# Kernel tuning notes

Measured on AMD Instinct MI355X. Metric: run time of the kernel, lower is better.

The kernel has to match this reference:

```python
import math
import jax, jax.numpy as jnp
import numpy as np

NUM_BUCKETS = 32
MAX_DISTANCE = 128
N_HEADS = 16
D_KV = 64


def _relative_position_bucket(rel_pos):
    # encoder (bidirectional) path of UMT5Attention._relative_position_bucket
    num_buckets = NUM_BUCKETS // 2
    rel_buckets = (rel_pos > 0).astype(jnp.int32) * num_buckets
    rel_pos = jnp.abs(rel_pos)
    max_exact = num_buckets // 2
    is_small = rel_pos < max_exact
    # clamp to 1 inside log only to avoid nan; those entries are masked by is_small
    rel_pos_large = max_exact + (
        jnp.log(jnp.maximum(rel_pos, 1).astype(jnp.float32) / max_exact)
        / math.log(MAX_DISTANCE / max_exact)
        * (num_buckets - max_exact)
    ).astype(jnp.int32)
    rel_pos_large = jnp.minimum(rel_pos_large, num_buckets - 1)
    return rel_buckets + jnp.where(is_small, rel_pos, rel_pos_large)


def compute_bias(rel_bias, q_len, k_len):
    ctx = jnp.arange(q_len, dtype=jnp.int32)[:, None]
    mem = jnp.arange(k_len, dtype=jnp.int32)[None, :]
    bkt = _relative_position_bucket(mem - ctx)          # [q, k]
    values = rel_bias[bkt]                               # [q, k, H]
    return jnp.transpose(values, (2, 0, 1))[None]        # [1, H, q, k]


def setup_inputs() -> dict:
    key = jax.random.key(0)
    ks = jax.random.split(key, 6)
    B, S, D = 2, 2048, 1024
    s = 1.0 / math.sqrt(D)
    return {
        "hidden_states": jax.random.normal(ks[0], (B, S, D), jnp.float32),
        "attention_mask": jnp.ones((B, S), jnp.int32),
        "Wq": jax.random.normal(ks[1], (D, D), jnp.float32) * s,
        "Wk": jax.random.normal(ks[2], (D, D), jnp.float32) * s,
        "Wv": jax.random.normal(ks[3], (D, D), jnp.float32) * s,
        "Wo": jax.random.normal(ks[4], (D, D), jnp.float32) * s,
        "rel_bias": jax.random.normal(ks[5], (NUM_BUCKETS, N_HEADS), jnp.float32),
    }


def reference(hidden_states, attention_mask, Wq, Wk, Wv, Wo, rel_bias):
    b, s, _ = hidden_states.shape
    n, c = N_HEADS, D_KV
    q = (hidden_states @ Wq).reshape(b, s, n, c)
    k = (hidden_states @ Wk).reshape(b, s, n, c)
    v = (hidden_states @ Wv).reshape(b, s, n, c)
    position_bias = compute_bias(rel_bias, s, s)          # [1, H, s, s]
    mask = attention_mask[:, None, None, :]               # [b, 1, 1, s]
    position_bias = jnp.where(mask == 0,
                              jnp.finfo(hidden_states.dtype).min,
                              position_bias)
    # T5-style: no 1/sqrt(d) query scaling
    attn = jnp.einsum('binc,bjnc->bnij', q, k) + position_bias
    attn = jax.nn.softmax(attn, axis=-1)
    o = jnp.einsum('bnij,bjnc->binc', attn, v).reshape(b, s, n * c)
    return o @ Wo
```

## Files before the change

### kernel.cpp

```cpp
#include <hip/hip_runtime.h>
#include <hip/hip_bf16.h>

#define NH 16
#define DC 64
#define SEQ 2048
#define BATCH 2
#define DM 1024
#define MTOT (BATCH*SEQ)

#define LOG2E 1.44269504f
#define SMAX_BOUND 48.0f

typedef unsigned short u16;
typedef unsigned int u32;
typedef __bf16 bf16x8 __attribute__((ext_vector_type(8)));
typedef float f32x4 __attribute__((ext_vector_type(4)));
typedef int i32x4 __attribute__((ext_vector_type(4)));
typedef unsigned u32x2v __attribute__((ext_vector_type(2)));

struct __attribute__((packed, aligned(4))) f4u { f32x4 v; };

__device__ __forceinline__ u16 f2bf(float f) {
    unsigned int x = __float_as_uint(f);
    unsigned int r = (x + 0x7fffu + ((x >> 16) & 1u)) >> 16;
    return (u16)r;
}
__device__ __forceinline__ u32 cvtpk(float a, float b) {
    u32 r;
    asm("v_cvt_pk_bf16_f32 %0, %1, %2" : "=v"(r) : "v"(a), "v"(b));
    return r;
}

__device__ __forceinline__ f32x4 mfma16(bf16x8 a, bf16x8 b, f32x4 c) {
    return __builtin_amdgcn_mfma_f32_16x16x32_bf16(a, b, c, 0, 0, 0);
}

__device__ __forceinline__ void glds(const u16* g, u16* l) {
    __builtin_amdgcn_global_load_lds(
        (const __attribute__((address_space(1))) void*)g,
        (__attribute__((address_space(3))) void*)l, 16, 0, 0);
}

__device__ __forceinline__ float psum32(float v) {
    u32x2v t = __builtin_amdgcn_permlane32_swap(__float_as_uint(v), __float_as_uint(v), false, false);
    return __uint_as_float(t.x) + __uint_as_float(t.y);
}
__device__ __forceinline__ float psum16(float v) {
    u32x2v t = __builtin_amdgcn_permlane16_swap(__float_as_uint(v), __float_as_uint(v), false, false);
    return __uint_as_float(t.x) + __uint_as_float(t.y);
}


__global__ void convert_hs(const float* __restrict__ src, u16* __restrict__ dst, int n4) {
    int idx = blockIdx.x * blockDim.x + threadIdx.x;
    int stride = gridDim.x * blockDim.x;
    for (int i = idx; i < n4; i += stride) {
        float4 v = reinterpret_cast<const float4*>(src)[i];
        uint2 o;
        o.x = (unsigned)f2bf(v.x) | ((unsigned)f2bf(v.y) << 16);
        o.y = (unsigned)f2bf(v.z) | ((unsigned)f2bf(v.w) << 16);
        reinterpret_cast<uint2*>(dst)[i] = o;
    }
}

__global__ void wtrans(const float* __restrict__ Wq, const float* __restrict__ Wk,
                       const float* __restrict__ Wv, const float* __restrict__ Wo,
                       u16* __restrict__ wT) {
    int z = blockIdx.z;
    const float* W = (z == 0) ? Wq : (z == 1) ? Wk : (z == 2) ? Wv : Wo;
    float sc = (z == 0) ? LOG2E : 1.0f;
    u16* WT = wT + (size_t)z * DM * DM;
    __shared__ float tile[32][33];
    int tx = threadIdx.x, ty = threadIdx.y;
    int kbase = blockIdx.y * 32, nbase = blockIdx.x * 32;
#pragma unroll
    for (int i = 0; i < 4; i++)
        tile[ty * 4 + i][tx] = W[(size_t)(kbase + ty * 4 + i) * DM + nbase + tx];
    __syncthreads();
#pragma unroll
    for (int i = 0; i < 4; i++)
        WT[(size_t)(nbase + ty * 4 + i) * DM + kbase + tx] = f2bf(tile[tx][ty * 4 + i] * sc);
}

__global__ void bias_table(const float* __restrict__ rel_bias, float* __restrict__ tab) {
    int idx = blockIdx.x * blockDim.x + threadIdx.x;
    if (idx >= NH * 2 * SEQ) return;
    int n = idx >> 12;
    int dpos = idx & 4095;
    int delta = dpos - 2048;
    int rb = (delta > 0) ? 16 : 0;
    int a = (delta < 0) ? -delta : delta;
    int ib;
    if (a < 8) {
        ib = a;
    } else {
        ib = 8 + (int)(logf((float)a / 8.0f) / logf(16.0f) * 8.0f);
        if (ib > 15) ib = 15;
    }
    tab[idx] = (rel_bias[(rb + ib) * NH + n] - SMAX_BOUND) * LOG2E;
}

__global__ __launch_bounds__(256) void vtrans(const u16* __restrict__ V, u16* __restrict__ VT) {
    int st = blockIdx.x;
    int hb = blockIdx.y;
    const u16* src = V + ((size_t)hb * SEQ + st * 64) * DC;
    u16* dst = VT + (size_t)hb * DC * SEQ + st * 64;
    __shared__ u16 t[64][65];
    int tid = threadIdx.x;
    int r = tid >> 2, c0 = (tid & 3) * 16;
    union { bf16x8 v; u16 s[8]; } a0, a1;
    a0.v = *reinterpret_cast<const bf16x8*>(src + (size_t)r * DC + c0);
    a1.v = *reinterpret_cast<const bf16x8*>(src + (size_t)r * DC + c0 + 8);
#pragma unroll
    for (int j = 0; j < 8; j++) { t[r][c0 + j] = a0.s[j]; t[r][c0 + 8 + j] = a1.s[j]; }
    __syncthreads();
    int c = tid >> 2, s0 = (tid & 3) * 16;
    union { bf16x8 v; u16 s[8]; } o0, o1;
#pragma unroll
    for (int j = 0; j < 8; j++) { o0.s[j] = t[s0 + j][c]; o1.s[j] = t[s0 + 8 + j][c]; }
    *reinterpret_cast<bf16x8*>(dst + (size_t)c * SEQ + s0)     = o0.v;
    *reinterpret_cast<bf16x8*>(dst + (size_t)c * SEQ + s0 + 8) = o1.v;
}


template<int MODE>
__global__ __launch_bounds__(256) void gemm_bt(
    const u16* __restrict__ A, const u16* __restrict__ BT,
    u16* __restrict__ qkvout, float* __restrict__ fout)
{
    const int NTILES = DM / 128;
    const int MTILES = MTOT / 128;
    __shared__ u16 As[128 * 32];
    __shared__ u16 Bs[128 * 32];

    int nb8 = gridDim.x >> 3;
    int bid = (blockIdx.x & 7) * nb8 + (blockIdx.x >> 3);

    int proj = 0, mt, nt;
    if (MODE == 0) {
        proj = bid / (MTILES * NTILES);
        int r = bid % (MTILES * NTILES);
        mt = r / NTILES; nt = r % NTILES;
    } else {
        mt = bid / NTILES; nt = bid % NTILES;
    }
    const u16* Bp = BT + (size_t)proj * DM * DM;
    int m0 = mt * 128, n0 = nt * 128;
    int tid = threadIdx.x;
    int lane = tid & 63, wid = tid >> 6;
    int wrow = (wid >> 1) * 64, wcol = (wid & 1) * 64;

    f32x4 acc[4][4] = {};

    int srow = lane >> 2;
    int skoff = (lane & 3) * 8;

    for (int k0 = 0; k0 < DM; k0 += 32) {
        __syncthreads();
#pragma unroll
        for (int t = 0; t < 2; t++) {
            int chunk = wid * 2 + t;
            int row = chunk * 16 + srow;
            glds(A + (size_t)(m0 + row) * DM + k0 + skoff, &As[chunk * 512]);
        }
#pragma unroll
        for (int t = 0; t < 2; t++) {
            int chunk = wid * 2 + t;
            int row = chunk * 16 + srow;
            glds(Bp + (size_t)(n0 + row) * DM + k0 + skoff, &Bs[chunk * 512]);
        }
        __syncthreads();

        int ko = (lane >> 4) * 8;
        bf16x8 af[4], bfr[4];
#pragma unroll
        for (int mi = 0; mi < 4; mi++)
            af[mi] = *reinterpret_cast<const bf16x8*>(&As[(wrow + mi * 16 + (lane & 15)) * 32 + ko]);
#pragma unroll
        for (int ni = 0; ni < 4; ni++)
            bfr[ni] = *reinterpret_cast<const bf16x8*>(&Bs[(wcol + ni * 16 + (lane & 15)) * 32 + ko]);
#pragma unroll
        for (int mi = 0; mi < 4; mi++)
#pragma unroll
            for (int ni = 0; ni < 4; ni++)
                acc[mi][ni] = mfma16(af[mi], bfr[ni], acc[mi][ni]);
    }

    int rbase = (lane >> 4) * 4;
    int cidx = lane & 15;
#pragma unroll
    for (int mi = 0; mi < 4; mi++) {
#pragma unroll
        for (int ni = 0; ni < 4; ni++) {
#pragma unroll
            for (int r = 0; r < 4; r++) {
                int gm = m0 + wrow + mi * 16 + rbase + r;
                int gn = n0 + wcol + ni * 16 + cidx;
                float v = acc[mi][ni][r];
                if (MODE == 0) {
                    int b = gm >> 11, s = gm & (SEQ - 1);
                    int h = gn >> 6, c = gn & 63;
                    size_t off = (((size_t)b * NH + h) * SEQ + s) * DC + c;
                    qkvout[(size_t)proj * MTOT * DM + off] = f2bf(v);
                } else {
                    fout[(size_t)gm * DM + gn] = v;
                }
            }
        }
    }
}


__global__ __launch_bounds__(256) void attn_kernel(
    const u16* __restrict__ Q, const u16* __restrict__ K, const u16* __restrict__ VT,
    const int* __restrict__ mask, const float* __restrict__ btab,
    u16* __restrict__ O)
{
    __shared__ u16 smem[16384];

    int wg = blockIdx.x;
    int sw = (wg & 7) * 64 + (wg >> 3);
    int qt = sw & 15;
    int bh = sw >> 4;
    int h = bh & 15, b = bh >> 4;

    int tid = threadIdx.x, lane = tid & 63, wid = tid >> 6;
    int q15 = lane & 15, hi = lane >> 4;

    const u16* Qp  = Q  + (((size_t)b * NH + h) * SEQ) * DC;
    const u16* Kp  = K  + (((size_t)b * NH + h) * SEQ) * DC;
    const u16* VTp = VT + ((size_t)b * NH + h) * DC * SEQ;

    int qb = qt * 128 + wid * 32;
    int iq0 = qb + q15;
    int iq1 = qb + 16 + q15;

    bf16x8 qf00 = *reinterpret_cast<const bf16x8*>(Qp + (size_t)iq0 * DC + hi * 8);
    bf16x8 qf01 = *reinterpret_cast<const bf16x8*>(Qp + (size_t)iq0 * DC + 32 + hi * 8);
    bf16x8 qf10 = *reinterpret_cast<const bf16x8*>(Qp + (size_t)iq1 * DC + hi * 8);
    bf16x8 qf11 = *reinterpret_cast<const bf16x8*>(Qp + (size_t)iq1 * DC + 32 + hi * 8);

    int n0 = (wid * 2 + 0) * 64 + lane;
    int n1 = (wid * 2 + 1) * 64 + lane;
    int rA = n0 >> 3, rB = n1 >> 3;
    const u16* gK0 = Kp  + (size_t)rA * DC + (((n0 & 7) ^ (rA & 7)) * 8);
    const u16* gK1 = Kp  + (size_t)rB * DC + (((n1 & 7) ^ (rB & 7)) * 8);
    const u16* gV0 = VTp + (size_t)rA * SEQ + (((n0 & 7) ^ (rA & 7)) * 8);
    const u16* gV1 = VTp + (size_t)rB * SEQ + (((n1 & 7) ^ (rB & 7)) * 8);

    int x0 = (hi)     ^ (q15 & 7);
    int x1 = (hi + 4) ^ (q15 & 7);

    const float* bp0 = btab + (size_t)h * 2 * SEQ + 2048 + hi * 4 - iq0;
    const float* bp1 = bp0 - 16;
    const int* mkp = mask + (size_t)b * SEQ + hi * 4;

    float l0 = 0.0f, l1 = 0.0f;
    f32x4 oacc[4][2] = {};

    glds(gK0, &smem[(wid * 2 + 0) * 512]);
    glds(gK1, &smem[(wid * 2 + 1) * 512]);
    glds(gV0, &smem[4096 + (wid * 2 + 0) * 512]);
    glds(gV1, &smem[4096 + (wid * 2 + 1) * 512]);

#pragma unroll 1
    for (int t = 0; t < SEQ / 64; t++) {
        u16* KsT = smem + ((t & 1) << 13);
        u16* VsT = KsT + 4096;
        int kt = t * 64;

        f32x4 bv0[4], bv1[4]; i32x4 mv4[4];
#pragma unroll
        for (int kf = 0; kf < 4; kf++) {
            bv0[kf] = reinterpret_cast<const f4u*>(bp0 + kt + kf * 16)->v;
            bv1[kf] = reinterpret_cast<const f4u*>(bp1 + kt + kf * 16)->v;
            mv4[kf] = *reinterpret_cast<const i32x4*>(mkp + kt + kf * 16);
        }

        if (t < SEQ / 64 - 1) {
            u16* KsN = smem + (((t + 1) & 1) << 13);
            int aK = (t + 1) * 64 * DC;
            int aV = (t + 1) * 64;
            glds(gK0 + aK, &KsN[(wid * 2 + 0) * 512]);
            glds(gK1 + aK, &KsN[(wid * 2 + 1) * 512]);
            glds(gV0 + aV, &KsN[4096 + (wid * 2 + 0) * 512]);
            glds(gV1 + aV, &KsN[4096 + (wid * 2 + 1) * 512]);
            asm volatile("s_waitcnt vmcnt(4)" ::: "memory");
        } else {
            asm volatile("s_waitcnt vmcnt(0)" ::: "memory");
        }
        asm volatile("s_barrier" ::: "memory");

        f32x4 s0[4], s1[4];
        __builtin_amdgcn_s_setprio(1);
#pragma unroll
        for (int kf = 0; kf < 4; kf++) {
            bf16x8 ka0 = *reinterpret_cast<const bf16x8*>(&KsT[(kf * 16 + q15) * 64 + x0 * 8]);
            bf16x8 ka1 = *reinterpret_cast<const bf16x8*>(&KsT[(kf * 16 + q15) * 64 + x1 * 8]);
            f32x4 z0 = {};
            z0 = mfma16(ka0, qf00, z0);
            z0 = mfma16(ka1, qf01, z0);
            s0[kf] = z0;
            f32x4 z1 = {};
            z1 = mfma16(ka0, qf10, z1);
            z1 = mfma16(ka1, qf11, z1);
            s1[kf] = z1;
        }
        __builtin_amdgcn_s_setprio(0);

#pragma unroll
        for (int kf = 0; kf < 4; kf++) {
#pragma unroll
            for (int r = 0; r < 4; r++) {
                bool mv = (mv4[kf][r] != 0);
                float sv0 = s0[kf][r] + (mv ? bv0[kf][r] : -1e30f);
                float sv1 = s1[kf][r] + (mv ? bv1[kf][r] : -1e30f);
                float p0 = exp2f(sv0);
                float p1 = exp2f(sv1);
                s0[kf][r] = p0; l0 += p0;
                s1[kf][r] = p1; l1 += p1;
            }
        }

        bf16x8 pa00, pa01, pa10, pa11;
        {
            u32 c00 = cvtpk(s0[0][0], s0[0][1]);
            u32 c01 = cvtpk(s0[0][2], s0[0][3]);
            u32 c10 = cvtpk(s0[1][0], s0[1][1]);
            u32 c11 = cvtpk(s0[1][2], s0[1][3]);
            u32 c20 = cvtpk(s0[2][0], s0[2][1]);
            u32 c21 = cvtpk(s0[2][2], s0[2][3]);
            u32 c30 = cvtpk(s0[3][0], s0[3][1]);
            u32 c31 = cvtpk(s0[3][2], s0[3][3]);
            u32x2v t0 = __builtin_amdgcn_permlane32_swap(c00, c10, false, false); c00 = t0.x; c10 = t0.y;
            u32x2v t1 = __builtin_amdgcn_permlane32_swap(c01, c11, false, false); c01 = t1.x; c11 = t1.y;
            u32x2v t2 = __builtin_amdgcn_permlane32_swap(c20, c30, false, false); c20 = t2.x; c30 = t2.y;
            u32x2v t3 = __builtin_amdgcn_permlane32_swap(c21, c31, false, false); c21 = t3.x; c31 = t3.y;
            u32x2v t4 = __builtin_amdgcn_permlane16_swap(c00, c10, false, false); c00 = t4.x; c10 = t4.y;
            u32x2v t5 = __builtin_amdgcn_permlane16_swap(c01, c11, false, false); c01 = t5.x; c11 = t5.y;
            u32x2v t6 = __builtin_amdgcn_permlane16_swap(c20, c30, false, false); c20 = t6.x; c30 = t6.y;
            u32x2v t7 = __builtin_amdgcn_permlane16_swap(c21, c31, false, false); c21 = t7.x; c31 = t7.y;
            union { u32 w[4]; bf16x8 v; } up0, up1;
            up0.w[0] = c00; up0.w[1] = c01; up0.w[2] = c10; up0.w[3] = c11;
            up1.w[0] = c20; up1.w[1] = c21; up1.w[2] = c30; up1.w[3] = c31;
            pa00 = up0.v; pa01 = up1.v;
        }
        {
            u32 c00 = cvtpk(s1[0][0], s1[0][1]);
            u32 c01 = cvtpk(s1[0][2], s1[0][3]);
            u32 c10 = cvtpk(s1[1][0], s1[1][1]);
            u32 c11 = cvtpk(s1[1][2], s1[1][3]);
            u32 c20 = cvtpk(s1[2][0], s1[2][1]);
            u32 c21 = cvtpk(s1[2][2], s1[2][3]);
            u32 c30 = cvtpk(s1[3][0], s1[3][1]);
            u32 c31 = cvtpk(s1[3][2], s1[3][3]);
            u32x2v t0 = __builtin_amdgcn_permlane32_swap(c00, c10, false, false); c00 = t0.x; c10 = t0.y;
            u32x2v t1 = __builtin_amdgcn_permlane32_swap(c01, c11, false, false); c01 = t1.x; c11 = t1.y;
            u32x2v t2 = __builtin_amdgcn_permlane32_swap(c20, c30, false, false); c20 = t2.x; c30 = t2.y;
            u32x2v t3 = __builtin_amdgcn_permlane32_swap(c21, c31, false, false); c21 = t3.x; c31 = t3.y;
            u32x2v t4 = __builtin_amdgcn_permlane16_swap(c00, c10, false, false); c00 = t4.x; c10 = t4.y;
            u32x2v t5 = __builtin_amdgcn_permlane16_swap(c01, c11, false, false); c01 = t5.x; c11 = t5.y;
            u32x2v t6 = __builtin_amdgcn_permlane16_swap(c20, c30, false, false); c20 = t6.x; c30 = t6.y;
            u32x2v t7 = __builtin_amdgcn_permlane16_swap(c21, c31, false, false); c21 = t7.x; c31 = t7.y;
            union { u32 w[4]; bf16x8 v; } up0, up1;
            up0.w[0] = c00; up0.w[1] = c01; up0.w[2] = c10; up0.w[3] = c11;
            up1.w[0] = c20; up1.w[1] = c21; up1.w[2] = c30; up1.w[3] = c31;
            pa10 = up0.v; pa11 = up1.v;
        }

        __builtin_amdgcn_s_setprio(1);
#pragma unroll
        for (int ci = 0; ci < 4; ci++) {
            bf16x8 v0 = *reinterpret_cast<const bf16x8*>(&VsT[(ci * 16 + q15) * 64 + x0 * 8]);
            bf16x8 v1 = *reinterpret_cast<const bf16x8*>(&VsT[(ci * 16 + q15) * 64 + x1 * 8]);
            oacc[ci][0] = mfma16(v0, pa00, oacc[ci][0]);
            oacc[ci][0] = mfma16(v1, pa01, oacc[ci][0]);
            oacc[ci][1] = mfma16(v0, pa10, oacc[ci][1]);
            oacc[ci][1] = mfma16(v1, pa11, oacc[ci][1]);
        }
        __builtin_amdgcn_s_setprio(0);

        asm volatile("s_barrier" ::: "memory");
    }

    float rl0 = 1.0f / psum16(psum32(l0));
    float rl1 = 1.0f / psum16(psum32(l1));
    __syncthreads();
    u16* Ot = smem;
#pragma unroll
    for (int ci = 0; ci < 4; ci++) {
        u32 w00 = cvtpk(oacc[ci][0][0] * rl0, oacc[ci][0][1] * rl0);
        u32 w01 = cvtpk(oacc[ci][0][2] * rl0, oacc[ci][0][3] * rl0);
        int base0 = (wid * 32 + q15) * 72 + ci * 16 + hi * 4;
        *reinterpret_cast<u32*>(&Ot[base0])     = w00;
        *reinterpret_cast<u32*>(&Ot[base0 + 2]) = w01;
        u32 w10 = cvtpk(oacc[ci][1][0] * rl1, oacc[ci][1][1] * rl1);
        u32 w11 = cvtpk(oacc[ci][1][2] * rl1, oacc[ci][1][3] * rl1);
        int base1 = (wid * 32 + 16 + q15) * 72 + ci * 16 + hi * 4;
        *reinterpret_cast<u32*>(&Ot[base1])     = w10;
        *reinterpret_cast<u32*>(&Ot[base1 + 2]) = w11;
    }
    __syncthreads();
    int row = tid >> 1, part = tid & 1;
    bf16x8 o0 = *reinterpret_cast<const bf16x8*>(&Ot[row * 72 + part * 32]);
    bf16x8 o1 = *reinterpret_cast<const bf16x8*>(&Ot[row * 72 + part * 32 + 8]);
    bf16x8 o2 = *reinterpret_cast<const bf16x8*>(&Ot[row * 72 + part * 32 + 16]);
    bf16x8 o3 = *reinterpret_cast<const bf16x8*>(&Ot[row * 72 + part * 32 + 24]);
    size_t ob = ((size_t)b * SEQ + qt * 128 + row) * DM + h * DC + part * 32;
    *reinterpret_cast<bf16x8*>(&O[ob])      = o0;
    *reinterpret_cast<bf16x8*>(&O[ob + 8])  = o1;
    *reinterpret_cast<bf16x8*>(&O[ob + 16]) = o2;
    *reinterpret_cast<bf16x8*>(&O[ob + 24]) = o3;
}


extern "C" void kernel_launch(void* const* d_in, const int* in_sizes, int n_in,
                              void* d_out, int out_size, void* d_ws, size_t ws_size,
                              hipStream_t stream) {
    const float* hs   = (const float*)d_in[0];
    const int*   mask = (const int*)d_in[1];
    const float* Wq   = (const float*)d_in[2];
    const float* Wk   = (const float*)d_in[3];
    const float* Wv   = (const float*)d_in[4];
    const float* Wo   = (const float*)d_in[5];
    const float* rb   = (const float*)d_in[6];

    char* ws = (char*)d_ws;
    u16* hsb  = (u16*)(ws);
    u16* wT   = (u16*)(ws + 8388608);
    u16* Qb   = (u16*)(ws + 16777216);
    u16* Ob   = (u16*)(ws + 41943040);
    float* btab = (float*)(ws + 50331648);
    float* out = (float*)d_out;

    u16* VT = hsb;

    convert_hs<<<2048, 256, 0, stream>>>(hs, hsb, MTOT * DM / 4);
    wtrans<<<dim3(32, 32, 4), dim3(32, 8), 0, stream>>>(Wq, Wk, Wv, Wo, wT);
    bias_table<<<256, 256, 0, stream>>>(rb, btab);
    gemm_bt<0><<<768, 256, 0, stream>>>(hsb, wT, Qb, nullptr);
    vtrans<<<dim3(32, 32), 256, 0, stream>>>(Qb + 2 * (size_t)MTOT * DM, VT);
    attn_kernel<<<512, 256, 0, stream>>>(
        Qb, Qb + (size_t)MTOT * DM, VT, mask, btab, Ob);
    gemm_bt<1><<<256, 256, 0, stream>>>(Ob, wT + 3 * (size_t)DM * DM, nullptr, out);
}
```

Baseline: 149.4 us.

## Fuse prep kernels, store QKV row-major, compute softmax denominator via MFMA

```diff
diff --git a/kernel.cpp b/kernel.cpp
--- a/kernel.cpp
+++ b/kernel.cpp
@@ -41,76 +41,72 @@
         (__attribute__((address_space(3))) void*)l, 16, 0, 0);
 }
 
-__device__ __forceinline__ float psum32(float v) {
-    u32x2v t = __builtin_amdgcn_permlane32_swap(__float_as_uint(v), __float_as_uint(v), false, false);
-    return __uint_as_float(t.x) + __uint_as_float(t.y);
-}
-__device__ __forceinline__ float psum16(float v) {
-    u32x2v t = __builtin_amdgcn_permlane16_swap(__float_as_uint(v), __float_as_uint(v), false, false);
-    return __uint_as_float(t.x) + __uint_as_float(t.y);
-}
-
-
-__global__ void convert_hs(const float* __restrict__ src, u16* __restrict__ dst, int n4) {
-    int idx = blockIdx.x * blockDim.x + threadIdx.x;
-    int stride = gridDim.x * blockDim.x;
-    for (int i = idx; i < n4; i += stride) {
-        float4 v = reinterpret_cast<const float4*>(src)[i];
-        uint2 o;
-        o.x = (unsigned)f2bf(v.x) | ((unsigned)f2bf(v.y) << 16);
-        o.y = (unsigned)f2bf(v.z) | ((unsigned)f2bf(v.w) << 16);
-        reinterpret_cast<uint2*>(dst)[i] = o;
-    }
-}
-
-__global__ void wtrans(const float* __restrict__ Wq, const float* __restrict__ Wk,
-                       const float* __restrict__ Wv, const float* __restrict__ Wo,
-                       u16* __restrict__ wT) {
-    int z = blockIdx.z;
-    const float* W = (z == 0) ? Wq : (z == 1) ? Wk : (z == 2) ? Wv : Wo;
-    float sc = (z == 0) ? LOG2E : 1.0f;
-    u16* WT = wT + (size_t)z * DM * DM;
-    __shared__ float tile[32][33];
-    int tx = threadIdx.x, ty = threadIdx.y;
-    int kbase = blockIdx.y * 32, nbase = blockIdx.x * 32;
-#pragma unroll
-    for (int i = 0; i < 4; i++)
-        tile[ty * 4 + i][tx] = W[(size_t)(kbase + ty * 4 + i) * DM + nbase + tx];
-    __syncthreads();
-#pragma unroll
-    for (int i = 0; i < 4; i++)
-        WT[(size_t)(nbase + ty * 4 + i) * DM + kbase + tx] = f2bf(tile[tx][ty * 4 + i] * sc);
-}
-
-__global__ void bias_table(const float* __restrict__ rel_bias, float* __restrict__ tab) {
-    int idx = blockIdx.x * blockDim.x + threadIdx.x;
-    if (idx >= NH * 2 * SEQ) return;
-    int n = idx >> 12;
-    int dpos = idx & 4095;
-    int delta = dpos - 2048;
-    int rb = (delta > 0) ? 16 : 0;
-    int a = (delta < 0) ? -delta : delta;
-    int ib;
-    if (a < 8) {
-        ib = a;
+
+__global__ __launch_bounds__(256) void prep_kernel(
+    const float* __restrict__ hs,
+    const float* __restrict__ Wq, const float* __restrict__ Wk,
+    const float* __restrict__ Wv, const float* __restrict__ Wo,
+    const float* __restrict__ rel_bias,
+    u16* __restrict__ hsb, u16* __restrict__ wT, float* __restrict__ btab)
+{
+    int bid = blockIdx.x, tid = threadIdx.x;
+    if (bid < 4096) {
+        int z = bid >> 10, rem = bid & 1023;
+        int by = rem >> 5, bx = rem & 31;
+        const float* W = (z == 0) ? Wq : (z == 1) ? Wk : (z == 2) ? Wv : Wo;
+        float sc = (z == 0) ? LOG2E : 1.0f;
+        u16* WT = wT + (size_t)z * DM * DM;
+        __shared__ float tile[32][33];
+        int tx = tid & 31, ty = tid >> 5;
+        int kbase = by * 32, nbase = bx * 32;
+#pragma unroll
+        for (int i = 0; i < 4; i++)
+            tile[ty * 4 + i][tx] = W[(size_t)(kbase + ty * 4 + i) * DM + nbase + tx];
+        __syncthreads();
+#pragma unroll
+        for (int i = 0; i < 4; i++)
+            WT[(size_t)(nbase + ty * 4 + i) * DM + kbase + tx] = f2bf(tile[tx][ty * 4 + i] * sc);
+    } else if (bid < 6144) {
+        int idx = (bid - 4096) * 256 + tid;
+        int stride = 2048 * 256;
+        int n4 = MTOT * DM / 4;
+        for (int i = idx; i < n4; i += stride) {
+            float4 v = reinterpret_cast<const float4*>(hs)[i];
+            uint2 o;
+            o.x = (unsigned)f2bf(v.x) | ((unsigned)f2bf(v.y) << 16);
+            o.y = (unsigned)f2bf(v.z) | ((unsigned)f2bf(v.w) << 16);
+            reinterpret_cast<uint2*>(hsb)[i] = o;
+        }
     } else {
-        ib = 8 + (int)(logf((float)a / 8.0f) / logf(16.0f) * 8.0f);
-        if (ib > 15) ib = 15;
-    }
-    tab[idx] = (rel_bias[(rb + ib) * NH + n] - SMAX_BOUND) * LOG2E;
+        int idx = (bid - 6144) * 256 + tid;
+        int n = idx >> 12;
+        int dpos = idx & 4095;
+        int delta = dpos - 2048;
+        int rb = (delta > 0) ? 16 : 0;
+        int a = (delta < 0) ? -delta : delta;
+        int ib;
+        if (a < 8) {
+            ib = a;
+        } else {
+            ib = 8 + (int)(logf((float)a / 8.0f) / logf(16.0f) * 8.0f);
+            if (ib > 15) ib = 15;
+        }
+        btab[idx] = (rel_bias[(rb + ib) * NH + n] - SMAX_BOUND) * LOG2E;
+    }
 }
 
 __global__ __launch_bounds__(256) void vtrans(const u16* __restrict__ V, u16* __restrict__ VT) {
     int st = blockIdx.x;
     int hb = blockIdx.y;
-    const u16* src = V + ((size_t)hb * SEQ + st * 64) * DC;
+    int b = hb >> 4, h = hb & 15;
+    const u16* src = V + (size_t)(b * SEQ + st * 64) * DM + h * 64;
     u16* dst = VT + (size_t)hb * DC * SEQ + st * 64;
     __shared__ u16 t[64][65];
     int tid = threadIdx.x;
     int r = tid >> 2, c0 = (tid & 3) * 16;
     union { bf16x8 v; u16 s[8]; } a0, a1;
-    a0.v = *reinterpret_cast<const bf16x8*>(src + (size_t)r * DC + c0);
-    a1.v = *reinterpret_cast<const bf16x8*>(src + (size_t)r * DC + c0 + 8);
+    a0.v = *reinterpret_cast<const bf16x8*>(src + (size_t)r * DM + c0);
+    a1.v = *reinterpret_cast<const bf16x8*>(src + (size_t)r * DM + c0 + 8);
 #pragma unroll
     for (int j = 0; j < 8; j++) { t[r][c0 + j] = a0.s[j]; t[r][c0 + 8 + j] = a1.s[j]; }
     __syncthreads();
@@ -188,23 +184,29 @@
 
     int rbase = (lane >> 4) * 4;
     int cidx = lane & 15;
-#pragma unroll
-    for (int mi = 0; mi < 4; mi++) {
-#pragma unroll
-        for (int ni = 0; ni < 4; ni++) {
+    if (MODE == 0) {
+        u16* op = qkvout + (size_t)proj * MTOT * DM
+                + (size_t)(m0 + wrow + rbase) * DM + (n0 + wcol + cidx);
+#pragma unroll
+        for (int mi = 0; mi < 4; mi++) {
 #pragma unroll
             for (int r = 0; r < 4; r++) {
-                int gm = m0 + wrow + mi * 16 + rbase + r;
-                int gn = n0 + wcol + ni * 16 + cidx;
-                float v = acc[mi][ni][r];
-                if (MODE == 0) {
-                    int b = gm >> 11, s = gm & (SEQ - 1);
-                    int h = gn >> 6, c = gn & 63;
-                    size_t off = (((size_t)b * NH + h) * SEQ + s) * DC + c;
-                    qkvout[(size_t)proj * MTOT * DM + off] = f2bf(v);
-                } else {
-                    fout[(size_t)gm * DM + gn] = v;
-                }
+                u16* rowp = op + (size_t)(mi * 16 + r) * DM;
+#pragma unroll
+                for (int ni = 0; ni < 4; ni++)
+                    rowp[ni * 16] = f2bf(acc[mi][ni][r]);
+            }
+        }
+    } else {
+        float* opf = fout + (size_t)(m0 + wrow + rbase) * DM + (n0 + wcol + cidx);
+#pragma unroll
+        for (int mi = 0; mi < 4; mi++) {
+#pragma unroll
+            for (int r = 0; r < 4; r++) {
+                float* rowp = opf + (size_t)(mi * 16 + r) * DM;
+#pragma unroll
+                for (int ni = 0; ni < 4; ni++)
+                    rowp[ni * 16] = acc[mi][ni][r];
             }
         }
     }
@@ -227,24 +229,24 @@
     int tid = threadIdx.x, lane = tid & 63, wid = tid >> 6;
     int q15 = lane & 15, hi = lane >> 4;
 
-    const u16* Qp  = Q  + (((size_t)b * NH + h) * SEQ) * DC;
-    const u16* Kp  = K  + (((size_t)b * NH + h) * SEQ) * DC;
+    const u16* Qp  = Q  + (size_t)b * SEQ * DM + h * 64;
+    const u16* Kp  = K  + (size_t)b * SEQ * DM + h * 64;
     const u16* VTp = VT + ((size_t)b * NH + h) * DC * SEQ;
 
     int qb = qt * 128 + wid * 32;
     int iq0 = qb + q15;
     int iq1 = qb + 16 + q15;
 
-    bf16x8 qf00 = *reinterpret_cast<const bf16x8*>(Qp + (size_t)iq0 * DC + hi * 8);
-    bf16x8 qf01 = *reinterpret_cast<const bf16x8*>(Qp + (size_t)iq0 * DC + 32 + hi * 8);
-    bf16x8 qf10 = *reinterpret_cast<const bf16x8*>(Qp + (size_t)iq1 * DC + hi * 8);
-    bf16x8 qf11 = *reinterpret_cast<const bf16x8*>(Qp + (size_t)iq1 * DC + 32 + hi * 8);
+    bf16x8 qf00 = *reinterpret_cast<const bf16x8*>(Qp + (size_t)iq0 * DM + hi * 8);
+    bf16x8 qf01 = *reinterpret_cast<const bf16x8*>(Qp + (size_t)iq0 * DM + 32 + hi * 8);
+    bf16x8 qf10 = *reinterpret_cast<const bf16x8*>(Qp + (size_t)iq1 * DM + hi * 8);
+    bf16x8 qf11 = *reinterpret_cast<const bf16x8*>(Qp + (size_t)iq1 * DM + 32 + hi * 8);
 
     int n0 = (wid * 2 + 0) * 64 + lane;
     int n1 = (wid * 2 + 1) * 64 + lane;
     int rA = n0 >> 3, rB = n1 >> 3;
-    const u16* gK0 = Kp  + (size_t)rA * DC + (((n0 & 7) ^ (rA & 7)) * 8);
-    const u16* gK1 = Kp  + (size_t)rB * DC + (((n1 & 7) ^ (rB & 7)) * 8);
+    const u16* gK0 = Kp  + (size_t)rA * DM + (((n0 & 7) ^ (rA & 7)) * 8);
+    const u16* gK1 = Kp  + (size_t)rB * DM + (((n1 & 7) ^ (rB & 7)) * 8);
     const u16* gV0 = VTp + (size_t)rA * SEQ + (((n0 & 7) ^ (rA & 7)) * 8);
     const u16* gV1 = VTp + (size_t)rB * SEQ + (((n1 & 7) ^ (rB & 7)) * 8);
 
@@ -255,8 +257,11 @@
     const float* bp1 = bp0 - 16;
     const int* mkp = mask + (size_t)b * SEQ + hi * 4;
 
-    float l0 = 0.0f, l1 = 0.0f;
+    bf16x8 ones;
+    { union { u32 w[4]; bf16x8 v; } u; u.w[0] = u.w[1] = u.w[2] = u.w[3] = 0x3f803f80u; ones = u.v; }
+
     f32x4 oacc[4][2] = {};
+    f32x4 lacc0 = {}, lacc1 = {};
 
     glds(gK0, &smem[(wid * 2 + 0) * 512]);
     glds(gK1, &smem[(wid * 2 + 1) * 512]);
@@ -279,7 +284,7 @@
 
         if (t < SEQ / 64 - 1) {
             u16* KsN = smem + (((t + 1) & 1) << 13);
-            int aK = (t + 1) * 64 * DC;
+            int aK = (t + 1) * 64 * DM;
             int aV = (t + 1) * 64;
             glds(gK0 + aK, &KsN[(wid * 2 + 0) * 512]);
             glds(gK1 + aK, &KsN[(wid * 2 + 1) * 512]);
@@ -315,10 +320,8 @@
                 bool mv = (mv4[kf][r] != 0);
                 float sv0 = s0[kf][r] + (mv ? bv0[kf][r] : -1e30f);
                 float sv1 = s1[kf][r] + (mv ? bv1[kf][r] : -1e30f);
-                float p0 = exp2f(sv0);
-                float p1 = exp2f(sv1);
-                s0[kf][r] = p0; l0 += p0;
-                s1[kf][r] = p1; l1 += p1;
+                s0[kf][r] = exp2f(sv0);
+                s1[kf][r] = exp2f(sv1);
             }
         }
 
@@ -368,6 +371,11 @@
             pa10 = up0.v; pa11 = up1.v;
         }
 
+        lacc0 = mfma16(ones, pa00, lacc0);
+        lacc0 = mfma16(ones, pa01, lacc0);
+        lacc1 = mfma16(ones, pa10, lacc1);
+        lacc1 = mfma16(ones, pa11, lacc1);
+
         __builtin_amdgcn_s_setprio(1);
 #pragma unroll
         for (int ci = 0; ci < 4; ci++) {
@@ -383,8 +391,8 @@
         asm volatile("s_barrier" ::: "memory");
     }
 
-    float rl0 = 1.0f / psum16(psum32(l0));
-    float rl1 = 1.0f / psum16(psum32(l1));
+    float rl0 = 1.0f / lacc0[0];
+    float rl1 = 1.0f / lacc1[0];
     __syncthreads();
     u16* Ot = smem;
 #pragma unroll
@@ -435,9 +443,7 @@
 
     u16* VT = hsb;
 
-    convert_hs<<<2048, 256, 0, stream>>>(hs, hsb, MTOT * DM / 4);
-    wtrans<<<dim3(32, 32, 4), dim3(32, 8), 0, stream>>>(Wq, Wk, Wv, Wo, wT);
-    bias_table<<<256, 256, 0, stream>>>(rb, btab);
+    prep_kernel<<<6400, 256, 0, stream>>>(hs, Wq, Wk, Wv, Wo, rb, hsb, wT, btab);
     gemm_bt<0><<<768, 256, 0, stream>>>(hsb, wT, Qb, nullptr);
     vtrans<<<dim3(32, 32), 256, 0, stream>>>(Qb + 2 * (size_t)MTOT * DM, VT);
     attn_kernel<<<512, 256, 0, stream>>>(
```

Measured after the change: 155.6 us. 4.1% more time.
